# Performance work log

Hardware: AMD Instinct MI355X
Metric: run time of the kernel (lower is better)

The kernel has to match this reference:

```python
import jax, jax.numpy as jnp
from jax import lax
import numpy as np

N_MACRO, HIDDEN, N_LAYERS, N_REGIMES, N_ASSETS = 16, 256, 2, 3, 32
VIX_THRESHOLD, DEFENSIVE_ALLOC, EPSILON = 30.0, 0.4, 1e-8
N_EQ = 24  # equities = assets[:24], defensive = assets[24:]
N_DEF = N_ASSETS - N_EQ
LN_EPS = 1e-5


def setup_inputs() -> dict:
    key = jax.random.key(0)
    ks = jax.random.split(key, 16)
    B, S = 128, 1024
    inp = {
        'macro_features': jax.random.normal(ks[0], (B, S, N_MACRO), jnp.float32),
        'vix_values': jax.random.uniform(ks[1], (B,), jnp.float32) * 60.0,  # some above threshold
    }
    k = 1.0 / np.sqrt(HIDDEN)
    def u(kk, shape):
        return jax.random.uniform(kk, shape, jnp.float32, -k, k)
    # layer 0
    inp['lstm_Wih0'] = u(ks[2], (4 * HIDDEN, N_MACRO))
    inp['lstm_Whh0'] = u(ks[3], (4 * HIDDEN, HIDDEN))
    inp['lstm_bih0'] = u(ks[4], (4 * HIDDEN,))
    inp['lstm_bhh0'] = u(ks[5], (4 * HIDDEN,))
    # layer 1
    inp['lstm_Wih1'] = u(ks[6], (4 * HIDDEN, HIDDEN))
    inp['lstm_Whh1'] = u(ks[7], (4 * HIDDEN, HIDDEN))
    inp['lstm_bih1'] = u(ks[8], (4 * HIDDEN,))
    inp['lstm_bhh1'] = u(ks[9], (4 * HIDDEN,))
    inp['ln_gamma'] = jnp.ones((HIDDEN,), jnp.float32)
    inp['ln_beta'] = jnp.zeros((HIDDEN,), jnp.float32)
    inp['logits_W'] = u(ks[10], (N_REGIMES, HIDDEN))
    inp['logits_b'] = u(ks[11], (N_REGIMES,))
    inp['risk_budgets'] = jax.random.normal(ks[12], (N_REGIMES, N_ASSETS), jnp.float32) * 0.01
    return inp


def _lstm_layer(x, Wih, Whh, bih, bhh):
    # x: [B,S,I] -> h sequence [B,S,H]
    B = x.shape[0]
    H = Whh.shape[1]
    pre = jnp.einsum('bsi,gi->bsg', x, Wih) + bih + bhh  # [B,S,4H]
    def step(carry, p):
        h, c = carry
        g = p + h @ Whh.T
        i, f, gg, o = jnp.split(g, 4, axis=-1)
        c = jax.nn.sigmoid(f) * c + jax.nn.sigmoid(i) * jnp.tanh(gg)
        h = jax.nn.sigmoid(o) * jnp.tanh(c)
        return (h, c), h
    init = (jnp.zeros((B, H), x.dtype), jnp.zeros((B, H), x.dtype))
    _, hs = lax.scan(step, init, jnp.swapaxes(pre, 0, 1))
    return jnp.swapaxes(hs, 0, 1)


def _vix_override(beta, vix_mask):
    # vectorized version of the per-sample override loop
    eq, df = beta[:, :N_EQ], beta[:, N_EQ:]
    cur_def = df.sum(-1)
    shortfall = DEFENSIVE_ALLOC - cur_def
    eq_total = eq.sum(-1)
    ratio = jnp.minimum(shortfall / jnp.maximum(eq_total, EPSILON), 0.8)
    apply = vix_mask & (shortfall > 0) & (eq_total > EPSILON)
    new_eq = eq * (1.0 - ratio)[:, None]
    new_df = df + (shortfall / N_DEF)[:, None]
    b2 = jnp.concatenate([new_eq, new_df], axis=-1)
    b = jnp.where(apply[:, None], b2, beta)
    b_norm = b / (b.sum(-1, keepdims=True) + EPSILON)
    return jnp.where(vix_mask[:, None], b_norm, beta)


def reference(macro_features, vix_values,
              lstm_Wih0, lstm_Whh0, lstm_bih0, lstm_bhh0,
              lstm_Wih1, lstm_Whh1, lstm_bih1, lstm_bhh1,
              ln_gamma, ln_beta, logits_W, logits_b, risk_budgets):
    h1 = _lstm_layer(macro_features, lstm_Wih0, lstm_Whh0, lstm_bih0, lstm_bhh0)
    h2 = _lstm_layer(h1, lstm_Wih1, lstm_Whh1, lstm_bih1, lstm_bhh1)
    h_last = h2[:, -1, :]  # [B,H]
    mu = h_last.mean(-1, keepdims=True)
    var = ((h_last - mu) ** 2).mean(-1, keepdims=True)
    h_norm = (h_last - mu) / jnp.sqrt(var + LN_EPS) * ln_gamma + ln_beta
    regime_probs = jax.nn.softmax(h_norm @ logits_W.T + logits_b, axis=-1)  # [B,K]
    budgets = jax.nn.softmax(risk_budgets, axis=-1)  # [K,P]
    beta = jnp.einsum('bk,kp->bp', regime_probs, budgets)
    vix_mask = vix_values >= VIX_THRESHOLD
    beta = _vix_override(beta, vix_mask)
    return beta, regime_probs
```

## Files before the change

### kernel.cpp

```cpp
#include <hip/hip_runtime.h>

#define B_  128
#define S_  1024
#define H_  256
#define NM_ 16

typedef short bf16x8 __attribute__((ext_vector_type(8)));
typedef float f32x4  __attribute__((ext_vector_type(4)));

__device__ __forceinline__ short f2bf(float f) {
    unsigned u = __builtin_bit_cast(unsigned, f);
    unsigned r = (u + 0x7FFFu + ((u >> 16) & 1u)) >> 16;
    return (short)r;
}
__device__ __forceinline__ bf16x8 zero8() {
    bf16x8 v;
    #pragma unroll
    for (int j = 0; j < 8; ++j) v[j] = 0;
    return v;
}
__device__ __forceinline__ float sigf(float x)  { return 1.0f / (1.0f + __expf(-x)); }
__device__ __forceinline__ float tanh_(float x) { return 1.0f - 2.0f / (1.0f + __expf(2.0f * x)); }
__device__ __forceinline__ void vm_drain() {
    asm volatile("s_waitcnt vmcnt(0)" ::: "memory");
}

__device__ __forceinline__ int cload_int(const int* p) {
    int r;
    asm volatile("global_load_dword %0, %1, off sc0 sc1\n\ts_waitcnt vmcnt(0)"
                 : "=v"(r) : "v"(p) : "memory");
    return r;
}
__device__ __forceinline__ void cstore_int(int* p, int v) {
    asm volatile("global_store_dword %0, %1, off sc0 sc1" :: "v"(p), "v"(v) : "memory");
}
__device__ __forceinline__ void cstore_short(short* p, int v) {
    asm volatile("global_store_short %0, %1, off sc0 sc1" :: "v"(p), "v"(v) : "memory");
}
__device__ __forceinline__ void cload8x16(const short* p, bf16x8* d) {
    int4 a0, a1, a2, a3, a4, a5, a6, a7;
    asm volatile(
        "global_load_dwordx4 %0, %8, off sc0 sc1\n\t"
        "global_load_dwordx4 %1, %8, off offset:64 sc0 sc1\n\t"
        "global_load_dwordx4 %2, %8, off offset:128 sc0 sc1\n\t"
        "global_load_dwordx4 %3, %8, off offset:192 sc0 sc1\n\t"
        "global_load_dwordx4 %4, %8, off offset:256 sc0 sc1\n\t"
        "global_load_dwordx4 %5, %8, off offset:320 sc0 sc1\n\t"
        "global_load_dwordx4 %6, %8, off offset:384 sc0 sc1\n\t"
        "global_load_dwordx4 %7, %8, off offset:448 sc0 sc1\n\t"
        "s_waitcnt vmcnt(0)"
        : "=&v"(a0), "=&v"(a1), "=&v"(a2), "=&v"(a3),
          "=&v"(a4), "=&v"(a5), "=&v"(a6), "=&v"(a7)
        : "v"(p) : "memory");
    d[0] = __builtin_bit_cast(bf16x8, a0); d[1] = __builtin_bit_cast(bf16x8, a1);
    d[2] = __builtin_bit_cast(bf16x8, a2); d[3] = __builtin_bit_cast(bf16x8, a3);
    d[4] = __builtin_bit_cast(bf16x8, a4); d[5] = __builtin_bit_cast(bf16x8, a5);
    d[6] = __builtin_bit_cast(bf16x8, a6); d[7] = __builtin_bit_cast(bf16x8, a7);
}

__global__ __launch_bounds__(256, 1) void lstm_kernel(
    const float* __restrict__ x,
    const float* __restrict__ Wih0, const float* __restrict__ Whh0,
    const float* __restrict__ bih0, const float* __restrict__ bhh0,
    const float* __restrict__ Wih1, const float* __restrict__ Whh1,
    const float* __restrict__ bih1, const float* __restrict__ bhh1,
    short* __restrict__ h1ring, short* __restrict__ h2ring,
    float* __restrict__ hlast,
    int* __restrict__ flags0, int* __restrict__ flags1)
{
    const int g    = blockIdx.x & 7;
    const int role = blockIdx.x >> 3;
    const int lane = threadIdx.x & 63;
    const int wv   = threadIdx.x >> 6;
    const int n    = lane & 15;
    const int quad = lane >> 4;

    int* fl0 = flags0 + (g * 4) * 32;
    int* fl1 = flags1 + (g * 4) * 32;

    if (role < 4) {
        const int q = role;
        const int hu_base = q * 64 + wv * 16;
        bf16x8 wf[4][9];
        float  bias[4];
        #pragma unroll
        for (int G = 0; G < 4; ++G) {
            int col = G * 256 + hu_base + n;
            bias[G] = bih0[col] + bhh0[col];
            #pragma unroll
            for (int kt = 0; kt < 8; ++kt) {
                const float* p = Whh0 + (long)col * H_ + kt * 32 + quad * 8;
                bf16x8 v;
                #pragma unroll
                for (int j = 0; j < 8; ++j) v[j] = f2bf(p[j]);
                wf[G][kt] = v;
            }
            bf16x8 v = zero8();
            if (quad < 2) {
                const float* p = Wih0 + (long)col * NM_ + quad * 8;
                #pragma unroll
                for (int j = 0; j < 8; ++j) v[j] = f2bf(p[j]);
            }
            wf[G][8] = v;
        }
        const int bRow = g * 16 + n;
        f32x4 c = {0.f, 0.f, 0.f, 0.f};
        for (int t = 0; t < S_; ++t) {
            bf16x8 xfrag = zero8();
            if (quad < 2) {
                const float* p = x + ((long)bRow * S_ + t) * NM_ + quad * 8;
                #pragma unroll
                for (int j = 0; j < 8; ++j) xfrag[j] = f2bf(p[j]);
            }
            if (threadIdx.x < 8) {
                const int* fp  = (threadIdx.x < 4) ? (fl0 + threadIdx.x * 32)
                                                   : (fl1 + (threadIdx.x - 4) * 32);
                const int  tgt = (threadIdx.x < 4) ? t : (t - 3);
                while (cload_int(fp) < tgt) __builtin_amdgcn_s_sleep(1);
            }
            __syncthreads();

            bf16x8 af[9];
            if (t > 0) {
                cload8x16(h1ring + (((long)((t - 1) & 3) * B_ + bRow) * H_) + quad * 8, af);
            } else {
                #pragma unroll
                for (int kt = 0; kt < 8; ++kt) af[kt] = zero8();
            }
            af[8] = xfrag;

            f32x4 acc[4];
            #pragma unroll
            for (int G = 0; G < 4; ++G) {
                acc[G][0] = bias[G]; acc[G][1] = bias[G];
                acc[G][2] = bias[G]; acc[G][3] = bias[G];
            }
            #pragma unroll
            for (int kt = 0; kt < 9; ++kt)
                #pragma unroll
                for (int G = 0; G < 4; ++G)
                    acc[G] = __builtin_amdgcn_mfma_f32_16x16x32_bf16(af[kt], wf[G][kt], acc[G], 0, 0, 0);
            #pragma unroll
            for (int r = 0; r < 4; ++r) {
                float iv = sigf(acc[0][r]);
                float fv = sigf(acc[1][r]);
                float gv = tanh_(acc[2][r]);
                float ov = sigf(acc[3][r]);
                c[r] = fv * c[r] + iv * gv;
                float hv = ov * tanh_(c[r]);
                int b = g * 16 + quad * 4 + r;
                cstore_short(h1ring + (((long)(t & 3) * B_ + b) * H_) + hu_base + n,
                             (int)(unsigned short)f2bf(hv));
            }
            vm_drain();
            __syncthreads();
            if (threadIdx.x == 0) cstore_int(fl0 + q * 32, t + 1);
        }
    } else {
        const int q = role - 4;
        const int hu_base = q * 64 + wv * 16;
        bf16x8 wf[4][16];
        float  bias[4];
        #pragma unroll
        for (int G = 0; G < 4; ++G) {
            int col = G * 256 + hu_base + n;
            bias[G] = bih1[col] + bhh1[col];
            #pragma unroll
            for (int kt = 0; kt < 8; ++kt) {
                const float* p = Whh1 + (long)col * H_ + kt * 32 + quad * 8;
                bf16x8 v;
                #pragma unroll
                for (int j = 0; j < 8; ++j) v[j] = f2bf(p[j]);
                wf[G][kt] = v;
            }
            #pragma unroll
            for (int kt = 0; kt < 8; ++kt) {
                const float* p = Wih1 + (long)col * H_ + kt * 32 + quad * 8;
                bf16x8 v;
                #pragma unroll
                for (int j = 0; j < 8; ++j) v[j] = f2bf(p[j]);
                wf[G][8 + kt] = v;
            }
        }
        const int bRow = g * 16 + n;
        f32x4 c = {0.f, 0.f, 0.f, 0.f};
        for (int t = 0; t < S_; ++t) {
            if (threadIdx.x < 8) {
                const int* fp  = (threadIdx.x < 4) ? (fl0 + threadIdx.x * 32)
                                                   : (fl1 + (threadIdx.x - 4) * 32);
                const int  tgt = (threadIdx.x < 4) ? (t + 1) : t;
                while (cload_int(fp) < tgt) __builtin_amdgcn_s_sleep(1);
            }
            __syncthreads();

            bf16x8 af[16];
            if (t > 0) {
                cload8x16(h2ring + ((long)bRow * 2 + ((t - 1) & 1)) * H_ + quad * 8, af);
            } else {
                #pragma unroll
                for (int kt = 0; kt < 8; ++kt) af[kt] = zero8();
            }
            cload8x16(h1ring + (((long)(t & 3) * B_ + bRow) * H_) + quad * 8, af + 8);

            f32x4 acc[4];
            #pragma unroll
            for (int G = 0; G < 4; ++G) {
                acc[G][0] = bias[G]; acc[G][1] = bias[G];
                acc[G][2] = bias[G]; acc[G][3] = bias[G];
            }
            #pragma unroll
            for (int kt = 0; kt < 16; ++kt)
                #pragma unroll
                for (int G = 0; G < 4; ++G)
                    acc[G] = __builtin_amdgcn_mfma_f32_16x16x32_bf16(af[kt], wf[G][kt], acc[G], 0, 0, 0);
            #pragma unroll
            for (int r = 0; r < 4; ++r) {
                float iv = sigf(acc[0][r]);
                float fv = sigf(acc[1][r]);
                float gv = tanh_(acc[2][r]);
                float ov = sigf(acc[3][r]);
                c[r] = fv * c[r] + iv * gv;
                float hv = ov * tanh_(c[r]);
                int b = g * 16 + quad * 4 + r;
                cstore_short(h2ring + ((long)b * 2 + (t & 1)) * H_ + hu_base + n,
                             (int)(unsigned short)f2bf(hv));
                if (t == S_ - 1) hlast[b * H_ + hu_base + n] = hv;
            }
            vm_drain();
            __syncthreads();
            if (threadIdx.x == 0) cstore_int(fl1 + q * 32, t + 1);
        }
    }
}

__device__ __forceinline__ float blockSum(float v, float* sbuf) {
    #pragma unroll
    for (int off = 32; off > 0; off >>= 1) v += __shfl_down(v, off, 64);
    __syncthreads();
    if ((threadIdx.x & 63) == 0) sbuf[threadIdx.x >> 6] = v;
    __syncthreads();
    return sbuf[0] + sbuf[1] + sbuf[2] + sbuf[3];
}

__global__ __launch_bounds__(256) void tail_kernel(
    const float* __restrict__ hlast, const float* __restrict__ gamma,
    const float* __restrict__ lnbeta, const float* __restrict__ Wl,
    const float* __restrict__ bl, const float* __restrict__ rb,
    const float* __restrict__ vix, float* __restrict__ out)
{
    __shared__ float sbuf[4];
    __shared__ float pr[3], mxs[3], dens[3];
    __shared__ float bvec[32];
    const int b   = blockIdx.x;
    const int tid = threadIdx.x;

    float v  = hlast[b * H_ + tid];
    float mu = blockSum(v, sbuf) * (1.0f / 256.0f);
    float d  = v - mu;
    float var = blockSum(d * d, sbuf) * (1.0f / 256.0f);
    float hn  = d * rsqrtf(var + 1e-5f) * gamma[tid] + lnbeta[tid];

    float l[3];
    #pragma unroll
    for (int k = 0; k < 3; ++k)
        l[k] = blockSum(hn * Wl[k * H_ + tid], sbuf) + bl[k];

    if (tid == 0) {
        float m  = fmaxf(l[0], fmaxf(l[1], l[2]));
        float e0 = __expf(l[0] - m), e1 = __expf(l[1] - m), e2 = __expf(l[2] - m);
        float dn = e0 + e1 + e2;
        pr[0] = e0 / dn; pr[1] = e1 / dn; pr[2] = e2 / dn;
    }
    if (tid < 3) {
        float m = -1e30f;
        for (int p = 0; p < 32; ++p) m = fmaxf(m, rb[tid * 32 + p]);
        float dn = 0.f;
        for (int p = 0; p < 32; ++p) dn += __expf(rb[tid * 32 + p] - m);
        mxs[tid] = m; dens[tid] = dn;
    }
    __syncthreads();
    if (tid < 32) {
        float bp = 0.f;
        #pragma unroll
        for (int k = 0; k < 3; ++k)
            bp += pr[k] * __expf(rb[k * 32 + tid] - mxs[k]) / dens[k];
        bvec[tid] = bp;
    }
    __syncthreads();
    if (tid == 0) {
        bool  mask = vix[b] >= 30.0f;
        float eq_total = 0.f, cur_def = 0.f;
        for (int p = 0; p < 24; ++p) eq_total += bvec[p];
        for (int p = 24; p < 32; ++p) cur_def += bvec[p];
        float shortfall = 0.4f - cur_def;
        float ratio = fminf(shortfall / fmaxf(eq_total, 1e-8f), 0.8f);
        bool  apply = mask && (shortfall > 0.0f) && (eq_total > 1e-8f);
        float bb[32]; float ssum = 0.f;
        for (int p = 0; p < 32; ++p) {
            float b2 = (p < 24) ? bvec[p] * (1.0f - ratio) : bvec[p] + shortfall * (1.0f / 8.0f);
            float bv = apply ? b2 : bvec[p];
            bb[p] = bv; ssum += bv;
        }
        float inv = 1.0f / (ssum + 1e-8f);
        for (int p = 0; p < 32; ++p)
            out[b * 32 + p] = mask ? bb[p] * inv : bvec[p];
        #pragma unroll
        for (int k = 0; k < 3; ++k)
            out[B_ * 32 + b * 3 + k] = pr[k];
    }
}

extern "C" void kernel_launch(void* const* d_in, const int* in_sizes, int n_in,
                              void* d_out, int out_size, void* d_ws, size_t ws_size,
                              hipStream_t stream)
{
    const float* x    = (const float*)d_in[0];
    const float* vix  = (const float*)d_in[1];
    const float* Wih0 = (const float*)d_in[2];
    const float* Whh0 = (const float*)d_in[3];
    const float* bih0 = (const float*)d_in[4];
    const float* bhh0 = (const float*)d_in[5];
    const float* Wih1 = (const float*)d_in[6];
    const float* Whh1 = (const float*)d_in[7];
    const float* bih1 = (const float*)d_in[8];
    const float* bhh1 = (const float*)d_in[9];
    const float* lng  = (const float*)d_in[10];
    const float* lnb  = (const float*)d_in[11];
    const float* Wl   = (const float*)d_in[12];
    const float* bl   = (const float*)d_in[13];
    const float* rb   = (const float*)d_in[14];
    float* out = (float*)d_out;

    char*  ws     = (char*)d_ws;
    short* h1ring = (short*)ws;
    short* h2ring = (short*)(ws + 262144);
    float* hlast  = (float*)(ws + 393216);
    int*   flags0 = (int*)(ws + 524288);
    int*   flags1 = (int*)(ws + 528384);

    hipMemsetAsync(ws + 524288, 0, 8192, stream);
    lstm_kernel<<<64, 256, 0, stream>>>(x, Wih0, Whh0, bih0, bhh0,
                                        Wih1, Whh1, bih1, bhh1,
                                        h1ring, h2ring, hlast, flags0, flags1);
    tail_kernel<<<128, 256, 0, stream>>>(hlast, lng, lnb, Wl, bl, rb, vix, out);
}
```

Measured before the change: 4.124 ms.

## Replace block barriers with per-wave tag polling and deepen h1 ring

Each wave now publishes its own progress tag and polls the 16 producer wave tags of both layers with a wave-wide __all check. This replaces the thread-0 spin plus __syncthreads handshake per block. The h1 ring buffer grows from 4 to 16 slots, so layer 0 can run up to 15 steps ahead of layer 1 and the two layers are less tightly coupled. The cost is more polling traffic to global memory and a larger workspace; a dependency mistake would show up as a race.

```diff
diff --git a/kernel.cpp b/kernel.cpp
--- a/kernel.cpp
+++ b/kernel.cpp
@@ -4,6 +4,7 @@
 #define S_  1024
 #define H_  256
 #define NM_ 16
+#define NEG_INF_TGT (-0x7FFFFFFF)
 
 typedef short bf16x8 __attribute__((ext_vector_type(8)));
 typedef float f32x4  __attribute__((ext_vector_type(4)));
@@ -58,6 +59,176 @@
     d[6] = __builtin_bit_cast(bf16x8, a6); d[7] = __builtin_bit_cast(bf16x8, a7);
 }
 
+__device__ __forceinline__ void tag_poll(const int* tagp, int tgt) {
+    for (;;) {
+        int tv = cload_int(tagp);
+        if (__all(tv >= tgt)) break;
+    }
+}
+
+__device__ void run_l0(const float* __restrict__ x, const float* __restrict__ Wih0,
+                       const float* __restrict__ Whh0, const float* __restrict__ bih0,
+                       const float* __restrict__ bhh0, short* __restrict__ h1ring,
+                       int* __restrict__ tags0, int* __restrict__ tags1, int g, int q)
+{
+    const int lane = threadIdx.x & 63, wv = threadIdx.x >> 6;
+    const int n = lane & 15, quad = lane >> 4;
+    const int hu_base = q * 64 + wv * 16;
+    bf16x8 wf[4][9];
+    float  bias[4];
+    #pragma unroll
+    for (int G = 0; G < 4; ++G) {
+        int col = G * 256 + hu_base + n;
+        bias[G] = bih0[col] + bhh0[col];
+        #pragma unroll
+        for (int kt = 0; kt < 8; ++kt) {
+            const float* p = Whh0 + (long)col * H_ + kt * 32 + quad * 8;
+            bf16x8 v;
+            #pragma unroll
+            for (int j = 0; j < 8; ++j) v[j] = f2bf(p[j]);
+            wf[G][kt] = v;
+        }
+        bf16x8 v = zero8();
+        if (quad < 2) {
+            const float* p = Wih0 + (long)col * NM_ + quad * 8;
+            #pragma unroll
+            for (int j = 0; j < 8; ++j) v[j] = f2bf(p[j]);
+        }
+        wf[G][8] = v;
+    }
+    const int bRow = g * 16 + n;
+    const int* tagp = (lane < 16) ? (tags0 + (g * 16 + lane) * 16)
+                    : (lane < 32) ? (tags1 + (g * 16 + lane - 16) * 16)
+                                  : (tags0 + g * 16 * 16);
+    int* mytag = tags0 + (g * 16 + q * 4 + wv) * 16;
+    f32x4 c = {0.f, 0.f, 0.f, 0.f};
+    for (int t = 0; t < S_; ++t) {
+        bf16x8 xfrag = zero8();
+        if (quad < 2) {
+            const float* p = x + ((long)bRow * S_ + t) * NM_ + quad * 8;
+            #pragma unroll
+            for (int j = 0; j < 8; ++j) xfrag[j] = f2bf(p[j]);
+        }
+        const int tgt = (lane < 16) ? t : ((lane < 32) ? (t - 15) : NEG_INF_TGT);
+        tag_poll(tagp, tgt);
+
+        bf16x8 af[9];
+        if (t > 0) {
+            cload8x16(h1ring + ((long)((t - 1) & 15) * B_ + bRow) * H_ + quad * 8, af);
+        } else {
+            #pragma unroll
+            for (int kt = 0; kt < 8; ++kt) af[kt] = zero8();
+        }
+        af[8] = xfrag;
+
+        f32x4 acc[4];
+        #pragma unroll
+        for (int G = 0; G < 4; ++G) {
+            acc[G][0] = bias[G]; acc[G][1] = bias[G];
+            acc[G][2] = bias[G]; acc[G][3] = bias[G];
+        }
+        #pragma unroll
+        for (int kt = 0; kt < 9; ++kt)
+            #pragma unroll
+            for (int G = 0; G < 4; ++G)
+                acc[G] = __builtin_amdgcn_mfma_f32_16x16x32_bf16(af[kt], wf[G][kt], acc[G], 0, 0, 0);
+        #pragma unroll
+        for (int r = 0; r < 4; ++r) {
+            float iv = sigf(acc[0][r]);
+            float fv = sigf(acc[1][r]);
+            float gv = tanh_(acc[2][r]);
+            float ov = sigf(acc[3][r]);
+            c[r] = fv * c[r] + iv * gv;
+            float hv = ov * tanh_(c[r]);
+            int b = g * 16 + quad * 4 + r;
+            cstore_short(h1ring + ((long)(t & 15) * B_ + b) * H_ + hu_base + n,
+                         (int)(unsigned short)f2bf(hv));
+        }
+        vm_drain();
+        if (lane == 0) cstore_int(mytag, t + 1);
+    }
+}
+
+__device__ void run_l1(const float* __restrict__ Wih1, const float* __restrict__ Whh1,
+                       const float* __restrict__ bih1, const float* __restrict__ bhh1,
+                       short* __restrict__ h1ring, short* __restrict__ h2ring,
+                       float* __restrict__ hlast,
+                       int* __restrict__ tags0, int* __restrict__ tags1, int g, int q)
+{
+    const int lane = threadIdx.x & 63, wv = threadIdx.x >> 6;
+    const int n = lane & 15, quad = lane >> 4;
+    const int hu_base = q * 64 + wv * 16;
+    bf16x8 wf[4][16];
+    float  bias[4];
+    #pragma unroll
+    for (int G = 0; G < 4; ++G) {
+        int col = G * 256 + hu_base + n;
+        bias[G] = bih1[col] + bhh1[col];
+        #pragma unroll
+        for (int kt = 0; kt < 8; ++kt) {
+            const float* p = Whh1 + (long)col * H_ + kt * 32 + quad * 8;
+            bf16x8 v;
+            #pragma unroll
+            for (int j = 0; j < 8; ++j) v[j] = f2bf(p[j]);
+            wf[G][kt] = v;
+        }
+        #pragma unroll
+        for (int kt = 0; kt < 8; ++kt) {
+            const float* p = Wih1 + (long)col * H_ + kt * 32 + quad * 8;
+            bf16x8 v;
+            #pragma unroll
+            for (int j = 0; j < 8; ++j) v[j] = f2bf(p[j]);
+            wf[G][8 + kt] = v;
+        }
+    }
+    const int bRow = g * 16 + n;
+    const int* tagp = (lane < 16) ? (tags0 + (g * 16 + lane) * 16)
+                    : (lane < 32) ? (tags1 + (g * 16 + lane - 16) * 16)
+                                  : (tags1 + g * 16 * 16);
+    int* mytag = tags1 + (g * 16 + q * 4 + wv) * 16;
+    f32x4 c = {0.f, 0.f, 0.f, 0.f};
+    for (int t = 0; t < S_; ++t) {
+        const int tgt = (lane < 16) ? (t + 1) : ((lane < 32) ? t : NEG_INF_TGT);
+        tag_poll(tagp, tgt);
+
+        bf16x8 af[16];
+        if (t > 0) {
+            cload8x16(h2ring + ((long)((t - 1) & 1) * B_ + bRow) * H_ + quad * 8, af);
+        } else {
+            #pragma unroll
+            for (int kt = 0; kt < 8; ++kt) af[kt] = zero8();
+        }
+        cload8x16(h1ring + ((long)(t & 15) * B_ + bRow) * H_ + quad * 8, af + 8);
+
+        f32x4 acc[4];
+        #pragma unroll
+        for (int G = 0; G < 4; ++G) {
+            acc[G][0] = bias[G]; acc[G][1] = bias[G];
+            acc[G][2] = bias[G]; acc[G][3] = bias[G];
+        }
+        #pragma unroll
+        for (int kt = 0; kt < 16; ++kt)
+            #pragma unroll
+            for (int G = 0; G < 4; ++G)
+                acc[G] = __builtin_amdgcn_mfma_f32_16x16x32_bf16(af[kt], wf[G][kt], acc[G], 0, 0, 0);
+        #pragma unroll
+        for (int r = 0; r < 4; ++r) {
+            float iv = sigf(acc[0][r]);
+            float fv = sigf(acc[1][r]);
+            float gv = tanh_(acc[2][r]);
+            float ov = sigf(acc[3][r]);
+            c[r] = fv * c[r] + iv * gv;
+            float hv = ov * tanh_(c[r]);
+            int b = g * 16 + quad * 4 + r;
+            cstore_short(h2ring + ((long)(t & 1) * B_ + b) * H_ + hu_base + n,
+                         (int)(unsigned short)f2bf(hv));
+            if (t == S_ - 1) hlast[b * H_ + hu_base + n] = hv;
+        }
+        vm_drain();
+        if (lane == 0) cstore_int(mytag, t + 1);
+    }
+}
+
 __global__ __launch_bounds__(256, 1) void lstm_kernel(
     const float* __restrict__ x,
     const float* __restrict__ Wih0, const float* __restrict__ Whh0,
@@ -66,171 +237,12 @@
     const float* __restrict__ bih1, const float* __restrict__ bhh1,
     short* __restrict__ h1ring, short* __restrict__ h2ring,
     float* __restrict__ hlast,
-    int* __restrict__ flags0, int* __restrict__ flags1)
+    int* __restrict__ tags0, int* __restrict__ tags1)
 {
     const int g    = blockIdx.x & 7;
     const int role = blockIdx.x >> 3;
-    const int lane = threadIdx.x & 63;
-    const int wv   = threadIdx.x >> 6;
-    const int n    = lane & 15;
-    const int quad = lane >> 4;
-
-    int* fl0 = flags0 + (g * 4) * 32;
-    int* fl1 = flags1 + (g * 4) * 32;
-
-    if (role < 4) {
-        const int q = role;
-        const int hu_base = q * 64 + wv * 16;
-        bf16x8 wf[4][9];
-        float  bias[4];
-        #pragma unroll
-        for (int G = 0; G < 4; ++G) {
-            int col = G * 256 + hu_base + n;
-            bias[G] = bih0[col] + bhh0[col];
-            #pragma unroll
-            for (int kt = 0; kt < 8; ++kt) {
-                const float* p = Whh0 + (long)col * H_ + kt * 32 + quad * 8;
-                bf16x8 v;
-                #pragma unroll
-                for (int j = 0; j < 8; ++j) v[j] = f2bf(p[j]);
-                wf[G][kt] = v;
-            }
-            bf16x8 v = zero8();
-            if (quad < 2) {
-                const float* p = Wih0 + (long)col * NM_ + quad * 8;
-                #pragma unroll
-                for (int j = 0; j < 8; ++j) v[j] = f2bf(p[j]);
-            }
-            wf[G][8] = v;
-        }
-        const int bRow = g * 16 + n;
-        f32x4 c = {0.f, 0.f, 0.f, 0.f};
-        for (int t = 0; t < S_; ++t) {
-            bf16x8 xfrag = zero8();
-            if (quad < 2) {
-                const float* p = x + ((long)bRow * S_ + t) * NM_ + quad * 8;
-                #pragma unroll
-                for (int j = 0; j < 8; ++j) xfrag[j] = f2bf(p[j]);
-            }
-            if (threadIdx.x < 8) {
-                const int* fp  = (threadIdx.x < 4) ? (fl0 + threadIdx.x * 32)
-                                                   : (fl1 + (threadIdx.x - 4) * 32);
-                const int  tgt = (threadIdx.x < 4) ? t : (t - 3);
-                while (cload_int(fp) < tgt) __builtin_amdgcn_s_sleep(1);
-            }
-            __syncthreads();
-
-            bf16x8 af[9];
-            if (t > 0) {
-                cload8x16(h1ring + (((long)((t - 1) & 3) * B_ + bRow) * H_) + quad * 8, af);
-            } else {
-                #pragma unroll
-                for (int kt = 0; kt < 8; ++kt) af[kt] = zero8();
-            }
-            af[8] = xfrag;
-
-            f32x4 acc[4];
-            #pragma unroll
-            for (int G = 0; G < 4; ++G) {
-                acc[G][0] = bias[G]; acc[G][1] = bias[G];
-                acc[G][2] = bias[G]; acc[G][3] = bias[G];
-            }
-            #pragma unroll
-            for (int kt = 0; kt < 9; ++kt)
-                #pragma unroll
-                for (int G = 0; G < 4; ++G)
-                    acc[G] = __builtin_amdgcn_mfma_f32_16x16x32_bf16(af[kt], wf[G][kt], acc[G], 0, 0, 0);
-            #pragma unroll
-            for (int r = 0; r < 4; ++r) {
-                float iv = sigf(acc[0][r]);
-                float fv = sigf(acc[1][r]);
-                float gv = tanh_(acc[2][r]);
-                float ov = sigf(acc[3][r]);
-                c[r] = fv * c[r] + iv * gv;
-                float hv = ov * tanh_(c[r]);
-                int b = g * 16 + quad * 4 + r;
-                cstore_short(h1ring + (((long)(t & 3) * B_ + b) * H_) + hu_base + n,
-                             (int)(unsigned short)f2bf(hv));
-            }
-            vm_drain();
-            __syncthreads();
-            if (threadIdx.x == 0) cstore_int(fl0 + q * 32, t + 1);
-        }
-    } else {
-        const int q = role - 4;
-        const int hu_base = q * 64 + wv * 16;
-        bf16x8 wf[4][16];
-        float  bias[4];
-        #pragma unroll
-        for (int G = 0; G < 4; ++G) {
-            int col = G * 256 + hu_base + n;
-            bias[G] = bih1[col] + bhh1[col];
-            #pragma unroll
-            for (int kt = 0; kt < 8; ++kt) {
-                const float* p = Whh1 + (long)col * H_ + kt * 32 + quad * 8;
-                bf16x8 v;
-                #pragma unroll
-                for (int j = 0; j < 8; ++j) v[j] = f2bf(p[j]);
-                wf[G][kt] = v;
-            }
-            #pragma unroll
-            for (int kt = 0; kt < 8; ++kt) {
-                const float* p = Wih1 + (long)col * H_ + kt * 32 + quad * 8;
-                bf16x8 v;
-                #pragma unroll
-                for (int j = 0; j < 8; ++j) v[j] = f2bf(p[j]);
-                wf[G][8 + kt] = v;
-            }
-        }
-        const int bRow = g * 16 + n;
-        f32x4 c = {0.f, 0.f, 0.f, 0.f};
-        for (int t = 0; t < S_; ++t) {
-            if (threadIdx.x < 8) {
-                const int* fp  = (threadIdx.x < 4) ? (fl0 + threadIdx.x * 32)
-                                                   : (fl1 + (threadIdx.x - 4) * 32);
-                const int  tgt = (threadIdx.x < 4) ? (t + 1) : t;
-                while (cload_int(fp) < tgt) __builtin_amdgcn_s_sleep(1);
-            }
-            __syncthreads();
-
-            bf16x8 af[16];
-            if (t > 0) {
-                cload8x16(h2ring + ((long)bRow * 2 + ((t - 1) & 1)) * H_ + quad * 8, af);
-            } else {
-                #pragma unroll
-                for (int kt = 0; kt < 8; ++kt) af[kt] = zero8();
-            }
-            cload8x16(h1ring + (((long)(t & 3) * B_ + bRow) * H_) + quad * 8, af + 8);
-
-            f32x4 acc[4];
-            #pragma unroll
-            for (int G = 0; G < 4; ++G) {
-                acc[G][0] = bias[G]; acc[G][1] = bias[G];
-                acc[G][2] = bias[G]; acc[G][3] = bias[G];
-            }
-            #pragma unroll
-            for (int kt = 0; kt < 16; ++kt)
-                #pragma unroll
-                for (int G = 0; G < 4; ++G)
-                    acc[G] = __builtin_amdgcn_mfma_f32_16x16x32_bf16(af[kt], wf[G][kt], acc[G], 0, 0, 0);
-            #pragma unroll
-            for (int r = 0; r < 4; ++r) {
-                float iv = sigf(acc[0][r]);
-                float fv = sigf(acc[1][r]);
-                float gv = tanh_(acc[2][r]);
-                float ov = sigf(acc[3][r]);
-                c[r] = fv * c[r] + iv * gv;
-                float hv = ov * tanh_(c[r]);
-                int b = g * 16 + quad * 4 + r;
-                cstore_short(h2ring + ((long)b * 2 + (t & 1)) * H_ + hu_base + n,
-                             (int)(unsigned short)f2bf(hv));
-                if (t == S_ - 1) hlast[b * H_ + hu_base + n] = hv;
-            }
-            vm_drain();
-            __syncthreads();
-            if (threadIdx.x == 0) cstore_int(fl1 + q * 32, t + 1);
-        }
-    }
+    if (role < 4) run_l0(x, Wih0, Whh0, bih0, bhh0, h1ring, tags0, tags1, g, role);
+    else          run_l1(Wih1, Whh1, bih1, bhh1, h1ring, h2ring, hlast, tags0, tags1, g, role - 4);
 }
 
 __device__ __forceinline__ float blockSum(float v, float* sbuf) {
@@ -333,14 +345,14 @@
 
     char*  ws     = (char*)d_ws;
     short* h1ring = (short*)ws;
-    short* h2ring = (short*)(ws + 262144);
-    float* hlast  = (float*)(ws + 393216);
-    int*   flags0 = (int*)(ws + 524288);
-    int*   flags1 = (int*)(ws + 528384);
-
-    hipMemsetAsync(ws + 524288, 0, 8192, stream);
+    short* h2ring = (short*)(ws + 1048576);
+    float* hlast  = (float*)(ws + 1179648);
+    int*   tags0  = (int*)(ws + 1310720);
+    int*   tags1  = (int*)(ws + 1318912);
+
+    hipMemsetAsync(ws + 1310720, 0, 16384, stream);
     lstm_kernel<<<64, 256, 0, stream>>>(x, Wih0, Whh0, bih0, bhh0,
                                         Wih1, Whh1, bih1, bhh1,
-                                        h1ring, h2ring, hlast, flags0, flags1);
+                                        h1ring, h2ring, hlast, tags0, tags1);
     tail_kernel<<<128, 256, 0, stream>>>(hlast, lng, lnb, Wl, bl, rb, vix, out);
 }
```

Result: slower. 4.822 ms (+16.9%).
